# Performance work log

Measured on AMD Instinct MI355X. Metric: run time of the kernel, lower is better.

The kernel has to match this reference:

```python
import jax, jax.numpy as jnp
import numpy as np

B, S, D, H = 2, 2048, 1024, 16
HD = D // H  # head_dim = 64


def setup_inputs() -> dict:
    key = jax.random.key(0)
    ks = jax.random.split(key, 6)
    scale = 0.02
    x = jax.random.normal(ks[0], (B, S, D), dtype=jnp.float32)
    Wq = jax.random.normal(ks[1], (D, D), dtype=jnp.float32) * scale
    Wk = jax.random.normal(ks[2], (D, D), dtype=jnp.float32) * scale
    Wv = jax.random.normal(ks[3], (D, D), dtype=jnp.float32) * scale
    Wo = jax.random.normal(ks[4], (D, D), dtype=jnp.float32) * scale
    bo = jnp.zeros((D,), dtype=jnp.float32)
    return {"x": x, "Wq": Wq, "Wk": Wk, "Wv": Wv, "Wo": Wo, "bo": bo}


def reference(x, Wq, Wk, Wv, Wo, bo):
    b, s, _ = x.shape
    # Linear projections (qkv_bias=False), split into heads: [b, h, s, hd]
    def split_heads(t):
        return t.reshape(b, s, H, HD).transpose(0, 2, 1, 3)
    q = split_heads(x @ Wq)
    k = split_heads(x @ Wk)
    v = split_heads(x @ Wv)
    # Scaled dot-product scores: [b, h, s, s]
    scores = jnp.einsum('bhqd,bhkd->bhqk', q, k) / jnp.sqrt(jnp.float32(HD))
    # Causal mask: triu(ones, diagonal=1) positions -> -inf
    causal = jnp.triu(jnp.ones((s, s), dtype=bool), k=1)
    scores = jnp.where(causal, -jnp.inf, scores)
    attn = jax.nn.softmax(scores, axis=-1)
    # dropout p=0.0 (eval-equivalent): identity
    ctx = jnp.einsum('bhqk,bhkd->bhqd', attn, v)  # [b, h, s, hd]
    ctx = ctx.transpose(0, 2, 1, 3).reshape(b, s, D)
    return ctx @ Wo + bo
```

## Files before the change

### kernel.cpp

```cpp
#include <hip/hip_runtime.h>
#include <math.h>

#define BB 2
#define SS 2048
#define DD 1024
#define HH 16
#define HD 64
#define MM (BB * SS)

typedef __bf16 bf16;
typedef __attribute__((ext_vector_type(8))) __bf16 bf16x8;
typedef __attribute__((ext_vector_type(4))) __bf16 bf16x4;
typedef __attribute__((ext_vector_type(4))) float f32x4;

__device__ __forceinline__ void gld_lds16(const void* g, void* l) {
    __builtin_amdgcn_global_load_lds(
        (const __attribute__((address_space(1))) void*)g,
        (__attribute__((address_space(3))) void*)l, 16, 0, 0);
}

__global__ __launch_bounds__(256) void prep(
    const float* __restrict__ x,
    const float* __restrict__ W0, const float* __restrict__ W1,
    const float* __restrict__ W2, const float* __restrict__ W3,
    bf16* __restrict__ xb, bf16* __restrict__ Wt)
{
    __shared__ float tile[32][33];
    const int z = blockIdx.z;
    if (z < 4) {
        const float* W = (z == 0) ? W0 : (z == 1) ? W1 : (z == 2) ? W2 : W3;
        bf16* O = Wt + (size_t)z * DD * DD;
        const int tx = threadIdx.x & 31, ty = threadIdx.x >> 5;
        const int k0 = blockIdx.y * 32, n0 = blockIdx.x * 32;
#pragma unroll
        for (int i = 0; i < 4; ++i)
            tile[ty + i * 8][tx] = W[(size_t)(k0 + ty + i * 8) * DD + n0 + tx];
        __syncthreads();
#pragma unroll
        for (int i = 0; i < 4; ++i)
            O[(size_t)(n0 + ty + i * 8) * DD + k0 + tx] = (bf16)tile[tx][ty + i * 8];
    } else {
        const int lb = (z - 4) * 1024 + blockIdx.y * 32 + blockIdx.x;
        const size_t i = ((size_t)lb * 256 + threadIdx.x) * 8;
        const float4 a = *(const float4*)(x + i);
        const float4 b = *(const float4*)(x + i + 4);
        bf16x8 o;
        o[0] = (bf16)a.x; o[1] = (bf16)a.y; o[2] = (bf16)a.z; o[3] = (bf16)a.w;
        o[4] = (bf16)b.x; o[5] = (bf16)b.y; o[6] = (bf16)b.z; o[7] = (bf16)b.w;
        *(bf16x8*)(xb + i) = o;
    }
}

__device__ __forceinline__ void mfma_core(
    const bf16* __restrict__ A, const bf16* __restrict__ Bt,
    int bm, int bn, int K, bf16* As, bf16* Bs, f32x4 (&acc)[4][4])
{
    const int t = threadIdx.x;
    const int w = t >> 6;
    const int l16 = t & 15, quad = (t >> 4) & 3;
    const int wr = w >> 1, wc = w & 1;
    const int arow = t >> 2;
    const int achk = (t & 3) << 3;

    const bf16* gA = A + (size_t)(bm + arow) * K + achk;
    const bf16* gB = Bt + (size_t)(bn + arow) * K + achk;
    bf16* lA = As + w * 512;
    bf16* lB = Bs + w * 512;

    for (int k0 = 0; k0 < K; k0 += 32) {
        gld_lds16(gA + k0, lA);
        gld_lds16(gA + (size_t)64 * K + k0, lA + 2048);
        gld_lds16(gB + k0, lB);
        gld_lds16(gB + (size_t)64 * K + k0, lB + 2048);
        __syncthreads();

        bf16x8 af[4], bv[4];
#pragma unroll
        for (int i = 0; i < 4; ++i) {
            af[i] = *(const bf16x8*)(As + (wr * 64 + i * 16 + l16) * 32 + quad * 8);
            bv[i] = *(const bf16x8*)(Bs + (wc * 64 + i * 16 + l16) * 32 + quad * 8);
        }
#pragma unroll
        for (int mi = 0; mi < 4; ++mi)
#pragma unroll
            for (int ni = 0; ni < 4; ++ni)
                acc[mi][ni] = __builtin_amdgcn_mfma_f32_16x16x32_bf16(
                    af[mi], bv[ni], acc[mi][ni], 0, 0, 0);
        __syncthreads();
    }
}

__global__ __launch_bounds__(256) void gemm_qkv(
    const bf16* __restrict__ xb, const bf16* __restrict__ Wt,
    bf16* __restrict__ Qb, bf16* __restrict__ Kb, bf16* __restrict__ Vb)
{
    __shared__ __align__(16) bf16 As[128 * 32];
    __shared__ __align__(16) bf16 Bs[128 * 32];
    const int bm = blockIdx.y * 128, bn = blockIdx.x * 128, z = blockIdx.z;

    f32x4 acc[4][4] = {};
    mfma_core(xb, Wt + (size_t)z * DD * DD, bm, bn, DD, As, Bs, acc);

    const int t = threadIdx.x;
    const int w = t >> 6, l16 = t & 15, quad = (t >> 4) & 3;
    const int wr = w >> 1, wc = w & 1;
    bf16* outp = (z == 0) ? Qb : (z == 1) ? Kb : Vb;

#pragma unroll
    for (int mi = 0; mi < 4; ++mi) {
#pragma unroll
        for (int ni = 0; ni < 4; ++ni) {
            const int col = bn + wc * 64 + ni * 16 + l16;
            const int h = col >> 6, hd = col & 63;
#pragma unroll
            for (int r = 0; r < 4; ++r) {
                const int row = bm + wr * 64 + mi * 16 + quad * 4 + r;
                const int b = row >> 11, s = row & (SS - 1);
                size_t addr;
                if (z < 2) addr = ((size_t)((b * HH + h) * SS + s)) * HD + hd;
                else       addr = ((size_t)((b * HH + h) * HD + hd)) * SS + s;
                outp[addr] = (bf16)acc[mi][ni][r];
            }
        }
    }
}

__global__ __launch_bounds__(256) void gemm_out(
    const bf16* __restrict__ ctx, const bf16* __restrict__ Wto,
    const float* __restrict__ bias, float* __restrict__ out)
{
    __shared__ __align__(16) bf16 As[128 * 32];
    __shared__ __align__(16) bf16 Bs[128 * 32];
    const int bm = blockIdx.y * 128, bn = blockIdx.x * 128;

    f32x4 acc[4][4] = {};
    mfma_core(ctx, Wto, bm, bn, DD, As, Bs, acc);

    const int t = threadIdx.x;
    const int w = t >> 6, l16 = t & 15, quad = (t >> 4) & 3;
    const int wr = w >> 1, wc = w & 1;

#pragma unroll
    for (int mi = 0; mi < 4; ++mi) {
#pragma unroll
        for (int ni = 0; ni < 4; ++ni) {
            const int col = bn + wc * 64 + ni * 16 + l16;
            const float b = bias[col];
#pragma unroll
            for (int r = 0; r < 4; ++r) {
                const int row = bm + wr * 64 + mi * 16 + quad * 4 + r;
                out[(size_t)row * DD + col] = acc[mi][ni][r] + b;
            }
        }
    }
}

#define PROWS 72
__global__ __launch_bounds__(256) void attn_flash(
    const bf16* __restrict__ Q, const bf16* __restrict__ K,
    const bf16* __restrict__ Vt, bf16* __restrict__ ctx)
{
    __shared__ __align__(16) bf16 Ks[2][64 * 64];
    __shared__ __align__(16) bf16 Vs[2][64 * 64];
    __shared__ __align__(16) bf16 Pl[4][16 * PROWS];

    const int t = threadIdx.x;
    const int w = t >> 6;
    const int lane = t & 63;
    const int l16 = lane & 15, quad = lane >> 4;

    const int L  = blockIdx.x;
    const int bh = L & 31;
    const int qg = 31 - (L >> 5);
    const int q0b = qg * 64;
    const int q0w = q0b + w * 16;

    const bf16* Qp = Q  + ((size_t)bh * SS + q0w) * HD;
    const bf16* Kp = K  + (size_t)bh * SS * HD;
    const bf16* Vp = Vt + (size_t)bh * HD * SS;
    bf16* Pw = &Pl[w][0];

    const bf16x8 bQ0 = *(const bf16x8*)(Qp + l16 * HD + quad * 8);
    const bf16x8 bQ1 = *(const bf16x8*)(Qp + l16 * HD + 32 + quad * 8);

    f32x4 accO[4] = {{0,0,0,0},{0,0,0,0},{0,0,0,0},{0,0,0,0}};
    float Lr = 0.f;
    const float cl2 = 0.125f * 1.44269504f;
    const int qrow = q0w + l16;

    const int r8 = lane >> 3, cs = lane & 7;
    const int nkt = qg + 1;

#pragma unroll
    for (int j = 0; j < 2; ++j) {
        const int region = w * 2 + j;
        const int row = region * 8 + r8;
        const int c = (cs - row) & 7;
        gld_lds16(Kp + (size_t)row * HD + c * 8, &Ks[0][region * 512]);
        gld_lds16(Vp + (size_t)row * SS + c * 8, &Vs[0][region * 512]);
    }

    for (int kt = 0; kt < nkt; ++kt) {
        const int kb = kt * 64;
        const int buf = kt & 1;
        __syncthreads();

        if (kt + 1 < nkt) {
            const int kb2 = kb + 64;
#pragma unroll
            for (int j = 0; j < 2; ++j) {
                const int region = w * 2 + j;
                const int row = region * 8 + r8;
                const int c = (cs - row) & 7;
                gld_lds16(Kp + (size_t)(kb2 + row) * HD + c * 8, &Ks[buf ^ 1][region * 512]);
                gld_lds16(Vp + (size_t)row * SS + kb2 + c * 8, &Vs[buf ^ 1][region * 512]);
            }
        }

        const bf16* Kbuf = &Ks[buf][0];
        const bf16* Vbuf = &Vs[buf][0];

        f32x4 St[4] = {{0,0,0,0},{0,0,0,0},{0,0,0,0},{0,0,0,0}};
#pragma unroll
        for (int mi = 0; mi < 4; ++mi) {
            const int row = mi * 16 + l16;
            const bf16x8 a0 = *(const bf16x8*)(Kbuf + row * 64 + ((quad + row) & 7) * 8);
            const bf16x8 a1 = *(const bf16x8*)(Kbuf + row * 64 + ((quad + 4 + row) & 7) * 8);
            St[mi] = __builtin_amdgcn_mfma_f32_16x16x32_bf16(a0, bQ0, St[mi], 0, 0, 0);
            St[mi] = __builtin_amdgcn_mfma_f32_16x16x32_bf16(a1, bQ1, St[mi], 0, 0, 0);
        }

        if (kb + 63 > q0w) {
#pragma unroll
            for (int mi = 0; mi < 4; ++mi)
#pragma unroll
                for (int r = 0; r < 4; ++r)
                    if (kb + mi * 16 + quad * 4 + r > qrow) St[mi][r] = -1e30f;
        }

        float rs = 0.f;
#pragma unroll
        for (int mi = 0; mi < 4; ++mi) {
            bf16x4 pk;
#pragma unroll
            for (int r = 0; r < 4; ++r) {
                const float p = exp2f(St[mi][r] * cl2);
                rs += p;
                pk[r] = (bf16)p;
            }
            *(bf16x4*)(Pw + l16 * PROWS + mi * 16 + quad * 4) = pk;
        }
        rs += __shfl_xor(rs, 16);
        rs += __shfl_xor(rs, 32);
        Lr += rs;

#pragma unroll
        for (int kc = 0; kc < 2; ++kc) {
            const bf16x8 bP = *(const bf16x8*)(Pw + l16 * PROWS + kc * 32 + quad * 8);
#pragma unroll
            for (int mi = 0; mi < 4; ++mi) {
                const int row = mi * 16 + l16;
                const bf16x8 aV = *(const bf16x8*)(
                    Vbuf + row * 64 + (((kc * 4 + quad) + row) & 7) * 8);
                accO[mi] = __builtin_amdgcn_mfma_f32_16x16x32_bf16(aV, bP, accO[mi], 0, 0, 0);
            }
        }
    }

    const float rinv = 1.0f / Lr;
    const int b = bh >> 4, h = bh & (HH - 1);
    bf16* op = ctx + ((size_t)(b * SS + q0w + l16)) * DD + h * HD;
#pragma unroll
    for (int mi = 0; mi < 4; ++mi) {
        bf16x4 o;
#pragma unroll
        for (int r = 0; r < 4; ++r) o[r] = (bf16)(accO[mi][r] * rinv);
        *(bf16x4*)(op + mi * 16 + quad * 4) = o;
    }
}

extern "C" void kernel_launch(void* const* d_in, const int* in_sizes, int n_in,
                              void* d_out, int out_size, void* d_ws, size_t ws_size,
                              hipStream_t stream)
{
    const float* x  = (const float*)d_in[0];
    const float* Wq = (const float*)d_in[1];
    const float* Wk = (const float*)d_in[2];
    const float* Wv = (const float*)d_in[3];
    const float* Wo = (const float*)d_in[4];
    const float* bo = (const float*)d_in[5];
    float* out = (float*)d_out;

    const size_t chunk = (size_t)MM * DD;
    bf16* xb  = (bf16*)d_ws;
    bf16* Wt  = xb + chunk;
    bf16* Qb  = Wt + 4 * (size_t)DD * DD;
    bf16* Kb  = Qb + chunk;
    bf16* Vb  = Kb + chunk;
    bf16* ctx = Vb + chunk;

    prep<<<dim3(32, 32, 6), dim3(256), 0, stream>>>(x, Wq, Wk, Wv, Wo, xb, Wt);

    gemm_qkv<<<dim3(DD / 128, MM / 128, 3), dim3(256), 0, stream>>>(xb, Wt, Qb, Kb, Vb);

    attn_flash<<<dim3(BB * HH * (SS / 64)), dim3(256), 0, stream>>>(Qb, Kb, Vb, ctx);

    gemm_out<<<dim3(DD / 128, MM / 128), dim3(256), 0, stream>>>(
        ctx, Wt + 3 * (size_t)DD * DD, bo, out);
}
```

Before: 190.6 us.

## Widen GEMM K-tile to 64 with swizzled LDS, vectorize epilogues, shrink attention KV tile

The GEMM core now loads 64-wide K slices into XOR-swizzled LDS, halving the number of barriers per K loop, and can swap MFMA operand order. With the swap, each lane holds 4 consecutive features, so the Q/K/V and output epilogues write bf16x4 or float4 vectors instead of scalars. The attention kernel switches to 32-key tiles with smaller LDS buffers and asks for 6 blocks per CU, trading more loop iterations for occupancy and finer causal skipping. Risks include added register pressure from the occupancy hint and more per-iteration overhead in attention.

```diff
diff --git a/kernel.cpp b/kernel.cpp
--- a/kernel.cpp
+++ b/kernel.cpp
@@ -51,6 +51,7 @@
     }
 }
 
+template<bool SWAP>
 __device__ __forceinline__ void mfma_core(
     const bf16* __restrict__ A, const bf16* __restrict__ Bt,
     int bm, int bn, int K, bf16* As, bf16* Bs, f32x4 (&acc)[4][4])
@@ -59,33 +60,39 @@
     const int w = t >> 6;
     const int l16 = t & 15, quad = (t >> 4) & 3;
     const int wr = w >> 1, wc = w & 1;
-    const int arow = t >> 2;
-    const int achk = (t & 3) << 3;
-
-    const bf16* gA = A + (size_t)(bm + arow) * K + achk;
-    const bf16* gB = Bt + (size_t)(bn + arow) * K + achk;
-    bf16* lA = As + w * 512;
-    bf16* lB = Bs + w * 512;
-
-    for (int k0 = 0; k0 < K; k0 += 32) {
-        gld_lds16(gA + k0, lA);
-        gld_lds16(gA + (size_t)64 * K + k0, lA + 2048);
-        gld_lds16(gB + k0, lB);
-        gld_lds16(gB + (size_t)64 * K + k0, lB + 2048);
+    const int r0 = t >> 3;
+    const int cs = t & 7;
+
+    for (int k0 = 0; k0 < K; k0 += 64) {
+#pragma unroll
+        for (int j = 0; j < 4; ++j) {
+            const int row = j * 32 + r0;
+            const int c = (cs - row) & 7;
+            gld_lds16(A  + (size_t)(bm + row) * K + k0 + c * 8,
+                      As + (j * 32 + w * 8) * 64);
+            gld_lds16(Bt + (size_t)(bn + row) * K + k0 + c * 8,
+                      Bs + (j * 32 + w * 8) * 64);
+        }
         __syncthreads();
 
-        bf16x8 af[4], bv[4];
-#pragma unroll
-        for (int i = 0; i < 4; ++i) {
-            af[i] = *(const bf16x8*)(As + (wr * 64 + i * 16 + l16) * 32 + quad * 8);
-            bv[i] = *(const bf16x8*)(Bs + (wc * 64 + i * 16 + l16) * 32 + quad * 8);
-        }
-#pragma unroll
-        for (int mi = 0; mi < 4; ++mi)
-#pragma unroll
-            for (int ni = 0; ni < 4; ++ni)
-                acc[mi][ni] = __builtin_amdgcn_mfma_f32_16x16x32_bf16(
-                    af[mi], bv[ni], acc[mi][ni], 0, 0, 0);
+#pragma unroll
+        for (int h = 0; h < 2; ++h) {
+            bf16x8 af[4], bv[4];
+#pragma unroll
+            for (int i = 0; i < 4; ++i) {
+                const int ra = wr * 64 + i * 16 + l16;
+                af[i] = *(const bf16x8*)(As + ra * 64 + (((h * 4 + quad) + ra) & 7) * 8);
+                const int rb = wc * 64 + i * 16 + l16;
+                bv[i] = *(const bf16x8*)(Bs + rb * 64 + (((h * 4 + quad) + rb) & 7) * 8);
+            }
+#pragma unroll
+            for (int mi = 0; mi < 4; ++mi)
+#pragma unroll
+                for (int ni = 0; ni < 4; ++ni)
+                    acc[mi][ni] = SWAP
+                        ? __builtin_amdgcn_mfma_f32_16x16x32_bf16(bv[mi], af[ni], acc[mi][ni], 0, 0, 0)
+                        : __builtin_amdgcn_mfma_f32_16x16x32_bf16(af[mi], bv[ni], acc[mi][ni], 0, 0, 0);
+        }
         __syncthreads();
     }
 }
@@ -94,32 +101,47 @@
     const bf16* __restrict__ xb, const bf16* __restrict__ Wt,
     bf16* __restrict__ Qb, bf16* __restrict__ Kb, bf16* __restrict__ Vb)
 {
-    __shared__ __align__(16) bf16 As[128 * 32];
-    __shared__ __align__(16) bf16 Bs[128 * 32];
+    __shared__ __align__(16) bf16 As[128 * 64];
+    __shared__ __align__(16) bf16 Bs[128 * 64];
     const int bm = blockIdx.y * 128, bn = blockIdx.x * 128, z = blockIdx.z;
-
-    f32x4 acc[4][4] = {};
-    mfma_core(xb, Wt + (size_t)z * DD * DD, bm, bn, DD, As, Bs, acc);
+    const bf16* Wz = Wt + (size_t)z * DD * DD;
 
     const int t = threadIdx.x;
     const int w = t >> 6, l16 = t & 15, quad = (t >> 4) & 3;
     const int wr = w >> 1, wc = w & 1;
-    bf16* outp = (z == 0) ? Qb : (z == 1) ? Kb : Vb;
-
-#pragma unroll
-    for (int mi = 0; mi < 4; ++mi) {
-#pragma unroll
-        for (int ni = 0; ni < 4; ++ni) {
-            const int col = bn + wc * 64 + ni * 16 + l16;
-            const int h = col >> 6, hd = col & 63;
-#pragma unroll
-            for (int r = 0; r < 4; ++r) {
-                const int row = bm + wr * 64 + mi * 16 + quad * 4 + r;
-                const int b = row >> 11, s = row & (SS - 1);
-                size_t addr;
-                if (z < 2) addr = ((size_t)((b * HH + h) * SS + s)) * HD + hd;
-                else       addr = ((size_t)((b * HH + h) * HD + hd)) * SS + s;
-                outp[addr] = (bf16)acc[mi][ni][r];
+
+    f32x4 acc[4][4] = {};
+    if (z < 2) {
+        mfma_core<true>(xb, Wz, bm, bn, DD, As, Bs, acc);
+        bf16* outp = (z == 0) ? Qb : Kb;
+#pragma unroll
+        for (int mi = 0; mi < 4; ++mi) {
+            const int feat = bn + wc * 64 + mi * 16 + quad * 4;
+            const int h = feat >> 6, hd = feat & 63;
+#pragma unroll
+            for (int ni = 0; ni < 4; ++ni) {
+                const int tok = bm + wr * 64 + ni * 16 + l16;
+                const int b = tok >> 11, s = tok & (SS - 1);
+                bf16x4 o;
+#pragma unroll
+                for (int r = 0; r < 4; ++r) o[r] = (bf16)acc[mi][ni][r];
+                *(bf16x4*)(outp + ((size_t)((b * HH + h) * SS + s)) * HD + hd) = o;
+            }
+        }
+    } else {
+        mfma_core<false>(xb, Wz, bm, bn, DD, As, Bs, acc);
+#pragma unroll
+        for (int mi = 0; mi < 4; ++mi) {
+            const int tok0 = bm + wr * 64 + mi * 16 + quad * 4;
+            const int b = tok0 >> 11, s0 = tok0 & (SS - 1);
+#pragma unroll
+            for (int ni = 0; ni < 4; ++ni) {
+                const int feat = bn + wc * 64 + ni * 16 + l16;
+                const int h = feat >> 6, hd = feat & 63;
+                bf16x4 o;
+#pragma unroll
+                for (int r = 0; r < 4; ++r) o[r] = (bf16)acc[mi][ni][r];
+                *(bf16x4*)(Vb + ((size_t)((b * HH + h) * HD + hd)) * SS + s0) = o;
             }
         }
     }
@@ -129,12 +151,12 @@
     const bf16* __restrict__ ctx, const bf16* __restrict__ Wto,
     const float* __restrict__ bias, float* __restrict__ out)
 {
-    __shared__ __align__(16) bf16 As[128 * 32];
-    __shared__ __align__(16) bf16 Bs[128 * 32];
+    __shared__ __align__(16) bf16 As[128 * 64];
+    __shared__ __align__(16) bf16 Bs[128 * 64];
     const int bm = blockIdx.y * 128, bn = blockIdx.x * 128;
 
     f32x4 acc[4][4] = {};
-    mfma_core(ctx, Wto, bm, bn, DD, As, Bs, acc);
+    mfma_core<true>(ctx, Wto, bm, bn, DD, As, Bs, acc);
 
     const int t = threadIdx.x;
     const int w = t >> 6, l16 = t & 15, quad = (t >> 4) & 3;
@@ -142,26 +164,28 @@
 
 #pragma unroll
     for (int mi = 0; mi < 4; ++mi) {
+        const int feat = bn + wc * 64 + mi * 16 + quad * 4;
+        const float4 bb = *(const float4*)(bias + feat);
 #pragma unroll
         for (int ni = 0; ni < 4; ++ni) {
-            const int col = bn + wc * 64 + ni * 16 + l16;
-            const float b = bias[col];
-#pragma unroll
-            for (int r = 0; r < 4; ++r) {
-                const int row = bm + wr * 64 + mi * 16 + quad * 4 + r;
-                out[(size_t)row * DD + col] = acc[mi][ni][r] + b;
-            }
-        }
-    }
-}
-
-#define PROWS 72
-__global__ __launch_bounds__(256) void attn_flash(
+            const int tok = bm + wr * 64 + ni * 16 + l16;
+            float4 o;
+            o.x = acc[mi][ni][0] + bb.x;
+            o.y = acc[mi][ni][1] + bb.y;
+            o.z = acc[mi][ni][2] + bb.z;
+            o.w = acc[mi][ni][3] + bb.w;
+            *(float4*)(out + (size_t)tok * DD + feat) = o;
+        }
+    }
+}
+
+#define PROWS 40
+__global__ __launch_bounds__(256, 6) void attn_flash(
     const bf16* __restrict__ Q, const bf16* __restrict__ K,
     const bf16* __restrict__ Vt, bf16* __restrict__ ctx)
 {
-    __shared__ __align__(16) bf16 Ks[2][64 * 64];
-    __shared__ __align__(16) bf16 Vs[2][64 * 64];
+    __shared__ __align__(16) bf16 Ks[2][32 * 64];
+    __shared__ __align__(16) bf16 Vs[2][64 * 32];
     __shared__ __align__(16) bf16 Pl[4][16 * PROWS];
 
     const int t = threadIdx.x;
@@ -188,41 +212,33 @@
     const float cl2 = 0.125f * 1.44269504f;
     const int qrow = q0w + l16;
 
-    const int r8 = lane >> 3, cs = lane & 7;
-    const int nkt = qg + 1;
-
-#pragma unroll
-    for (int j = 0; j < 2; ++j) {
-        const int region = w * 2 + j;
-        const int row = region * 8 + r8;
-        const int c = (cs - row) & 7;
-        gld_lds16(Kp + (size_t)row * HD + c * 8, &Ks[0][region * 512]);
-        gld_lds16(Vp + (size_t)row * SS + c * 8, &Vs[0][region * 512]);
-    }
+    const int krow = w * 8 + (lane >> 3), kcs = lane & 7;
+    const int kc_g = (kcs - krow) & 7;
+    const int vrow = w * 16 + (lane >> 2), vcs = lane & 3;
+    const int vc_g = (vcs - vrow) & 3;
+
+    const int nkt = 2 * qg + 2;
+
+    gld_lds16(Kp + (size_t)krow * HD + kc_g * 8, &Ks[0][w * 512]);
+    gld_lds16(Vp + (size_t)vrow * SS + vc_g * 8, &Vs[0][w * 512]);
 
     for (int kt = 0; kt < nkt; ++kt) {
-        const int kb = kt * 64;
+        const int kb = kt * 32;
         const int buf = kt & 1;
         __syncthreads();
 
         if (kt + 1 < nkt) {
-            const int kb2 = kb + 64;
-#pragma unroll
-            for (int j = 0; j < 2; ++j) {
-                const int region = w * 2 + j;
-                const int row = region * 8 + r8;
-                const int c = (cs - row) & 7;
-                gld_lds16(Kp + (size_t)(kb2 + row) * HD + c * 8, &Ks[buf ^ 1][region * 512]);
-                gld_lds16(Vp + (size_t)row * SS + kb2 + c * 8, &Vs[buf ^ 1][region * 512]);
-            }
+            const int kb2 = kb + 32;
+            gld_lds16(Kp + (size_t)(kb2 + krow) * HD + kc_g * 8, &Ks[buf ^ 1][w * 512]);
+            gld_lds16(Vp + (size_t)vrow * SS + kb2 + vc_g * 8, &Vs[buf ^ 1][w * 512]);
         }
 
         const bf16* Kbuf = &Ks[buf][0];
         const bf16* Vbuf = &Vs[buf][0];
 
-        f32x4 St[4] = {{0,0,0,0},{0,0,0,0},{0,0,0,0},{0,0,0,0}};
-#pragma unroll
-        for (int mi = 0; mi < 4; ++mi) {
+        f32x4 St[2] = {{0,0,0,0},{0,0,0,0}};
+#pragma unroll
+        for (int mi = 0; mi < 2; ++mi) {
             const int row = mi * 16 + l16;
             const bf16x8 a0 = *(const bf16x8*)(Kbuf + row * 64 + ((quad + row) & 7) * 8);
             const bf16x8 a1 = *(const bf16x8*)(Kbuf + row * 64 + ((quad + 4 + row) & 7) * 8);
@@ -230,9 +246,9 @@
             St[mi] = __builtin_amdgcn_mfma_f32_16x16x32_bf16(a1, bQ1, St[mi], 0, 0, 0);
         }
 
-        if (kb + 63 > q0w) {
-#pragma unroll
-            for (int mi = 0; mi < 4; ++mi)
+        if (kb + 31 > q0w) {
+#pragma unroll
+            for (int mi = 0; mi < 2; ++mi)
 #pragma unroll
                 for (int r = 0; r < 4; ++r)
                     if (kb + mi * 16 + quad * 4 + r > qrow) St[mi][r] = -1e30f;
@@ -240,7 +256,7 @@
 
         float rs = 0.f;
 #pragma unroll
-        for (int mi = 0; mi < 4; ++mi) {
+        for (int mi = 0; mi < 2; ++mi) {
             bf16x4 pk;
 #pragma unroll
             for (int r = 0; r < 4; ++r) {
@@ -254,16 +270,12 @@
         rs += __shfl_xor(rs, 32);
         Lr += rs;
 
-#pragma unroll
-        for (int kc = 0; kc < 2; ++kc) {
-            const bf16x8 bP = *(const bf16x8*)(Pw + l16 * PROWS + kc * 32 + quad * 8);
-#pragma unroll
-            for (int mi = 0; mi < 4; ++mi) {
-                const int row = mi * 16 + l16;
-                const bf16x8 aV = *(const bf16x8*)(
-                    Vbuf + row * 64 + (((kc * 4 + quad) + row) & 7) * 8);
-                accO[mi] = __builtin_amdgcn_mfma_f32_16x16x32_bf16(aV, bP, accO[mi], 0, 0, 0);
-            }
+        const bf16x8 bP = *(const bf16x8*)(Pw + l16 * PROWS + quad * 8);
+#pragma unroll
+        for (int mi = 0; mi < 4; ++mi) {
+            const int row = mi * 16 + l16;
+            const bf16x8 aV = *(const bf16x8*)(Vbuf + row * 32 + ((quad + row) & 3) * 8);
+            accO[mi] = __builtin_amdgcn_mfma_f32_16x16x32_bf16(aV, bP, accO[mi], 0, 0, 0);
         }
     }
 
```

Result: slower. 205.4 us (+7.8%).
